# Kernel optimization log

Measured on AMD Instinct MI355X. Metric: run time of the kernel, lower is better.

## Reference

```python
import jax, jax.numpy as jnp
import numpy as np

B, Hh, Ww, D = 16, 32, 32, 1024
NH, HD = 16, 64
S = Hh * Ww


def _rotate_pairwise(x):
    # (..., d) -> pairwise rotation: (x0,x1,x2,x3,...) -> (-x1,x0,-x3,x2,...)
    x = x.reshape(*x.shape[:-1], -1, 2)
    x1, x2 = x[..., 0], x[..., 1]
    return jnp.stack((-x2, x1), axis=-1).reshape(*x.shape[:-2], -1)


def setup_inputs() -> dict:
    key = jax.random.key(0)
    ks = jax.random.split(key, 12)
    s = 1.0 / np.sqrt(D)
    return {
        "hidden_states": jax.random.normal(ks[0], (B, Hh, Ww, D), jnp.float32),
        "cos": jax.random.uniform(ks[1], (S, HD), jnp.float32, -1.0, 1.0),
        "sin": jax.random.uniform(ks[2], (S, HD), jnp.float32, -1.0, 1.0),
        "Wq": jax.random.normal(ks[3], (D, D), jnp.float32) * s,
        "bq": jnp.zeros((D,), jnp.float32),
        "Wk": jax.random.normal(ks[4], (D, D), jnp.float32) * s,
        "bk": jnp.zeros((D,), jnp.float32),
        "Wv": jax.random.normal(ks[5], (D, D), jnp.float32) * s,
        "bv": jnp.zeros((D,), jnp.float32),
        "Wo": jax.random.normal(ks[6], (D, D), jnp.float32) * s,
        "bo": jnp.zeros((D,), jnp.float32),
    }


def reference(hidden_states, cos, sin, Wq, bq, Wk, bk, Wv, bv, Wo, bo):
    b, h, w, d = hidden_states.shape
    seq = h * w
    x = hidden_states.reshape(b, seq, d)
    # QKV projections -> (b, heads, seq, head_dim)
    def proj(W, bias):
        y = x @ W.T + bias
        return y.reshape(b, seq, NH, HD).transpose(0, 2, 1, 3)
    q, k, v = proj(Wq, bq), proj(Wk, bk), proj(Wv, bv)
    # RoPE in fp32; cos/sin (seq, head_dim) broadcast over (b, heads)
    qf = q.astype(jnp.float32)
    kf = k.astype(jnp.float32)
    q = (qf * cos + _rotate_pairwise(qf) * sin).astype(q.dtype)
    k = (kf * cos + _rotate_pairwise(kf) * sin).astype(k.dtype)
    # SDPA
    scale = HD ** -0.5
    scores = jnp.einsum("bhqd,bhkd->bhqk", q, k) * scale
    attn = jax.nn.softmax(scores, axis=-1)
    out = jnp.einsum("bhqk,bhkd->bhqd", attn, v)
    out = out.transpose(0, 2, 1, 3).reshape(b, h, w, d)
    return out @ Wo.T + bo
```

## Files before the change

kernel.cpp:

```cpp
#include <hip/hip_runtime.h>
#include <hip/hip_bf16.h>
#include <stdint.h>

#define Bb 16
#define Ss 1024
#define Dd 1024
#define NHh 16
#define HDd 64
#define Mm 16384

typedef _Float16 half8 __attribute__((ext_vector_type(8)));
typedef float f32x4 __attribute__((ext_vector_type(4)));

__device__ __forceinline__ void gload_lds16(const _Float16* g, _Float16* l) {
  auto* gp = (const __attribute__((address_space(1))) unsigned int*)(g);
  auto* lp = (__attribute__((address_space(3))) unsigned int*)(l);
  __builtin_amdgcn_global_load_lds(gp, lp, 16, 0, 0);
}

__global__ void cast_all(const float* __restrict__ x,
                         const float* __restrict__ wq, const float* __restrict__ wk,
                         const float* __restrict__ wv, const float* __restrict__ wo,
                         _Float16* __restrict__ xh, _Float16* __restrict__ wcat) {
  const long NX = (long)Mm * Dd / 4;
  const long NW = (long)Dd * Dd / 4;
  long c = (long)blockIdx.x * blockDim.x + threadIdx.x;
  const float* src;
  _Float16* dst;
  long o;
  if (c < NX) {
    src = x; o = c; dst = xh;
  } else {
    long cw = c - NX;
    int m = (int)(cw / NW);
    o = cw - (long)m * NW;
    src = (m == 0) ? wq : (m == 1) ? wk : (m == 2) ? wv : wo;
    dst = wcat + (long)m * (Dd * Dd);
  }
  float4 v = reinterpret_cast<const float4*>(src)[o];
  _Float16 h[4] = {(_Float16)v.x, (_Float16)v.y, (_Float16)v.z, (_Float16)v.w};
  reinterpret_cast<uint64_t*>(dst)[o] = *reinterpret_cast<uint64_t*>(h);
}

template <int EPI>
__global__ __launch_bounds__(256, 2) void gemm_nt(
    const _Float16* __restrict__ A, const _Float16* __restrict__ Bm,
    _Float16* __restrict__ qo, _Float16* __restrict__ ko, _Float16* __restrict__ vo,
    const float* __restrict__ bq, const float* __restrict__ bk, const float* __restrict__ bv,
    const float* __restrict__ cosp, const float* __restrict__ sinp,
    float* __restrict__ outp, const float* __restrict__ bo) {
  __shared__ __align__(16) _Float16 As[128 * 32];
  __shared__ __align__(16) _Float16 Bs[128 * 32];
  const int t = threadIdx.x;
  const int w = t >> 6, l = t & 63;
  const int g = l >> 4, ln = l & 15;
  const int wr = w >> 1, wc = w & 1;
  const long rowbase = (long)blockIdx.y * 128;
  const long colbase = (long)blockIdx.x * 128;
  const _Float16* Arow0 = A + rowbase * Dd;
  const _Float16* Brow0 = Bm + colbase * Dd;

  f32x4 acc[4][4];
#pragma unroll
  for (int i = 0; i < 4; ++i)
#pragma unroll
    for (int j = 0; j < 4; ++j) acc[i][j] = f32x4{0.f, 0.f, 0.f, 0.f};

  for (int kt = 0; kt < 32; ++kt) {
    const int kof = kt * 32;
#pragma unroll
    for (int h = 0; h < 2; ++h) {
      int chunk = t + h * 256;
      int r = chunk >> 2;
      int cc = (chunk & 3) * 8;
      gload_lds16(Arow0 + (long)r * Dd + kof + cc, &As[chunk * 8]);
      gload_lds16(Brow0 + (long)r * Dd + kof + cc, &Bs[chunk * 8]);
    }
    __syncthreads();
    half8 af[4], bf[4];
#pragma unroll
    for (int i = 0; i < 4; ++i) {
      af[i] = *reinterpret_cast<const half8*>(&As[(wr * 64 + i * 16 + ln) * 32 + g * 8]);
      bf[i] = *reinterpret_cast<const half8*>(&Bs[(wc * 64 + i * 16 + ln) * 32 + g * 8]);
    }
#pragma unroll
    for (int i = 0; i < 4; ++i)
#pragma unroll
      for (int j = 0; j < 4; ++j)
        acc[i][j] = __builtin_amdgcn_mfma_f32_16x16x32_f16(af[i], bf[j], acc[i][j], 0, 0, 0);
    __syncthreads();
  }

  if (EPI == 0) {
#pragma unroll
    for (int j = 0; j < 4; ++j) {
      long n = colbase + wc * 64 + j * 16 + ln;
      int mat = (int)(n >> 10);
      int col = (int)(n & 1023);
      int hh = col >> 6, hd = col & 63;
      float bias = (mat == 0) ? bq[col] : (mat == 1) ? bk[col] : bv[col];
      _Float16* dst = (mat == 0) ? qo : (mat == 1) ? ko : vo;
#pragma unroll
      for (int i = 0; i < 4; ++i) {
#pragma unroll
        for (int r = 0; r < 4; ++r) {
          long row = rowbase + wr * 64 + i * 16 + g * 4 + r;
          int b = (int)(row >> 10), s = (int)(row & 1023);
          float val = acc[i][j][r] + bias;
          if (mat < 2) {
            float part = __shfl_xor(val, 1);
            float cv = cosp[s * HDd + hd];
            float sv = sinp[s * HDd + hd];
            val = val * cv + ((hd & 1) ? part : -part) * sv;
          }
          dst[((long)(b * NHh + hh) * Ss + s) * HDd + hd] = (_Float16)val;
        }
      }
    }
  } else {
#pragma unroll
    for (int j = 0; j < 4; ++j) {
      long n = colbase + wc * 64 + j * 16 + ln;
      float bias = bo[n];
#pragma unroll
      for (int i = 0; i < 4; ++i)
#pragma unroll
        for (int r = 0; r < 4; ++r) {
          long row = rowbase + wr * 64 + i * 16 + g * 4 + r;
          outp[row * Dd + n] = acc[i][j][r] + bias;
        }
    }
  }
}

__global__ __launch_bounds__(256, 2) void attn(
    const _Float16* __restrict__ Q, const _Float16* __restrict__ K,
    const _Float16* __restrict__ V, _Float16* __restrict__ O) {
  __shared__ __align__(16) _Float16 Ks[64 * 72];
  __shared__ __align__(16) _Float16 Vt[64 * 72];
  __shared__ __align__(16) _Float16 Ps[4 * 16 * 72];
  const int t = threadIdx.x;
  const int w = t >> 6, l = t & 63;
  const int g = l >> 4, ln = l & 15;
  const int pair = blockIdx.y;
  const int qbase = blockIdx.x * 64;
  const long pbase = (long)pair * Ss * HDd;
  const float scale = 0.125f;

  half8 qf[2];
  {
    long qr = qbase + w * 16 + ln;
    const _Float16* qp = Q + pbase + qr * HDd + g * 8;
    qf[0] = *reinterpret_cast<const half8*>(qp);
    qf[1] = *reinterpret_cast<const half8*>(qp + 32);
  }

  float m_i = -1e30f, l_i = 0.0f;
  f32x4 acc_o[4];
#pragma unroll
  for (int c = 0; c < 4; ++c) acc_o[c] = f32x4{0.f, 0.f, 0.f, 0.f};

  for (int kt = 0; kt < 16; ++kt) {
#pragma unroll
    for (int h2 = 0; h2 < 2; ++h2) {
      int chunk = t + h2 * 256;
      int r = chunk >> 3;
      int cc = (chunk & 7) * 8;
      const _Float16* kp = K + pbase + (long)(kt * 64 + r) * HDd + cc;
      half8 kv = *reinterpret_cast<const half8*>(kp);
      *reinterpret_cast<half8*>(&Ks[r * 72 + cc]) = kv;
      const _Float16* vp = V + pbase + (long)(kt * 64 + r) * HDd + cc;
      half8 vv = *reinterpret_cast<const half8*>(vp);
#pragma unroll
      for (int jj = 0; jj < 8; ++jj) Vt[(cc + jj) * 72 + r] = vv[jj];
    }
    __syncthreads();

    f32x4 accs[4];
#pragma unroll
    for (int c = 0; c < 4; ++c) {
      half8 kf0 = *reinterpret_cast<const half8*>(&Ks[(c * 16 + ln) * 72 + g * 8]);
      half8 kf1 = *reinterpret_cast<const half8*>(&Ks[(c * 16 + ln) * 72 + 32 + g * 8]);
      f32x4 a = f32x4{0.f, 0.f, 0.f, 0.f};
      a = __builtin_amdgcn_mfma_f32_16x16x32_f16(kf0, qf[0], a, 0, 0, 0);
      a = __builtin_amdgcn_mfma_f32_16x16x32_f16(kf1, qf[1], a, 0, 0, 0);
      accs[c] = a;
    }

    float pv[16];
    float pmax = -1e30f;
#pragma unroll
    for (int c = 0; c < 4; ++c)
#pragma unroll
      for (int r = 0; r < 4; ++r) {
        float sv = accs[c][r] * scale;
        pv[c * 4 + r] = sv;
        pmax = fmaxf(pmax, sv);
      }
    pmax = fmaxf(pmax, __shfl_xor(pmax, 16));
    pmax = fmaxf(pmax, __shfl_xor(pmax, 32));
    float m_new = fmaxf(m_i, pmax);
    float alpha = __expf(m_i - m_new);
    float tsum = 0.0f;
#pragma unroll
    for (int z = 0; z < 16; ++z) {
      float e = __expf(pv[z] - m_new);
      pv[z] = e;
      tsum += e;
    }
    tsum += __shfl_xor(tsum, 16);
    tsum += __shfl_xor(tsum, 32);
    l_i = l_i * alpha + tsum;
    m_i = m_new;

    float alr[4];
#pragma unroll
    for (int r = 0; r < 4; ++r) alr[r] = __shfl(alpha, g * 4 + r);
#pragma unroll
    for (int c = 0; c < 4; ++c)
#pragma unroll
      for (int r = 0; r < 4; ++r) acc_o[c][r] *= alr[r];

    _Float16* prow = &Ps[(w * 16 + ln) * 72];
#pragma unroll
    for (int c = 0; c < 4; ++c) {
      _Float16 p4[4] = {(_Float16)pv[c * 4 + 0], (_Float16)pv[c * 4 + 1],
                        (_Float16)pv[c * 4 + 2], (_Float16)pv[c * 4 + 3]};
      *reinterpret_cast<uint2*>(&prow[c * 16 + g * 4]) = *reinterpret_cast<uint2*>(p4);
    }

#pragma unroll
    for (int kh = 0; kh < 2; ++kh) {
      half8 pf = *reinterpret_cast<const half8*>(&Ps[(w * 16 + ln) * 72 + kh * 32 + g * 8]);
#pragma unroll
      for (int c = 0; c < 4; ++c) {
        half8 vf = *reinterpret_cast<const half8*>(&Vt[(c * 16 + ln) * 72 + kh * 32 + g * 8]);
        acc_o[c] = __builtin_amdgcn_mfma_f32_16x16x32_f16(pf, vf, acc_o[c], 0, 0, 0);
      }
    }
    __syncthreads();
  }

  const int b = pair >> 4, hh = pair & 15;
  float linv[4];
#pragma unroll
  for (int r = 0; r < 4; ++r) linv[r] = 1.0f / __shfl(l_i, g * 4 + r);
#pragma unroll
  for (int c = 0; c < 4; ++c)
#pragma unroll
    for (int r = 0; r < 4; ++r) {
      int s = qbase + w * 16 + g * 4 + r;
      long addr = ((long)(b * Ss + s)) * Dd + hh * HDd + c * 16 + ln;
      O[addr] = (_Float16)(acc_o[c][r] * linv[r]);
    }
}

extern "C" void kernel_launch(void* const* d_in, const int* in_sizes, int n_in,
                              void* d_out, int out_size, void* d_ws, size_t ws_size,
                              hipStream_t stream) {
  (void)in_sizes; (void)n_in; (void)out_size; (void)ws_size;
  const float* x    = (const float*)d_in[0];
  const float* cosp = (const float*)d_in[1];
  const float* sinp = (const float*)d_in[2];
  const float* Wq   = (const float*)d_in[3];
  const float* bq   = (const float*)d_in[4];
  const float* Wk   = (const float*)d_in[5];
  const float* bk   = (const float*)d_in[6];
  const float* Wv   = (const float*)d_in[7];
  const float* bv   = (const float*)d_in[8];
  const float* Wo   = (const float*)d_in[9];
  const float* bo   = (const float*)d_in[10];
  float* out = (float*)d_out;

  char* ws = (char*)d_ws;
  _Float16* xh   = (_Float16*)(ws);
  _Float16* wcat = (_Float16*)(ws + 33554432);
  _Float16* Qb   = (_Float16*)(ws + 41943040);
  _Float16* Kb   = (_Float16*)(ws + 75497472);
  _Float16* Vb   = (_Float16*)(ws + 109051904);

  cast_all<<<dim3(20480), dim3(256), 0, stream>>>(x, Wq, Wk, Wv, Wo, xh, wcat);

  gemm_nt<0><<<dim3(24, 128), dim3(256), 0, stream>>>(
      xh, wcat, Qb, Kb, Vb, bq, bk, bv, cosp, sinp, (float*)nullptr, (const float*)nullptr);

  attn<<<dim3(16, 256), dim3(256), 0, stream>>>(Qb, Kb, Vb, xh);

  gemm_nt<1><<<dim3(8, 128), dim3(256), 0, stream>>>(
      xh, wcat + (long)3072 * 1024, (_Float16*)nullptr, (_Float16*)nullptr, (_Float16*)nullptr,
      (const float*)nullptr, (const float*)nullptr, (const float*)nullptr,
      (const float*)nullptr, (const float*)nullptr, out, bo);
}
```

Measured before the change: 589.6 us.

## Write V pre-transposed from QKV GEMM and use exp2 softmax in attention

The QKV projection epilogue now stores V in a head-dim-major (transposed) layout with packed 4-element stores, so the attention kernel can load V tiles into shared memory with vector stores instead of scalar transposing scatters. Softmax also folds log2(e) into the scale and uses the hardware exp2 directly. This trades strided global writes in the GEMM epilogue for cheaper LDS fills in the attention inner loop.

```diff
diff --git a/kernel.cpp b/kernel.cpp
--- a/kernel.cpp
+++ b/kernel.cpp
@@ -17,6 +17,8 @@
   auto* lp = (__attribute__((address_space(3))) unsigned int*)(l);
   __builtin_amdgcn_global_load_lds(gp, lp, 16, 0, 0);
 }
+
+__device__ __forceinline__ float fexp2(float x) { return __builtin_amdgcn_exp2f(x); }
 
 __global__ void cast_all(const float* __restrict__ x,
                          const float* __restrict__ wq, const float* __restrict__ wk,
@@ -99,21 +101,32 @@
       int col = (int)(n & 1023);
       int hh = col >> 6, hd = col & 63;
       float bias = (mat == 0) ? bq[col] : (mat == 1) ? bk[col] : bv[col];
-      _Float16* dst = (mat == 0) ? qo : (mat == 1) ? ko : vo;
-#pragma unroll
-      for (int i = 0; i < 4; ++i) {
-#pragma unroll
-        for (int r = 0; r < 4; ++r) {
-          long row = rowbase + wr * 64 + i * 16 + g * 4 + r;
-          int b = (int)(row >> 10), s = (int)(row & 1023);
-          float val = acc[i][j][r] + bias;
-          if (mat < 2) {
+      if (mat < 2) {
+        _Float16* dst = (mat == 0) ? qo : ko;
+#pragma unroll
+        for (int i = 0; i < 4; ++i) {
+#pragma unroll
+          for (int r = 0; r < 4; ++r) {
+            long row = rowbase + wr * 64 + i * 16 + g * 4 + r;
+            int b = (int)(row >> 10), s = (int)(row & 1023);
+            float val = acc[i][j][r] + bias;
             float part = __shfl_xor(val, 1);
             float cv = cosp[s * HDd + hd];
             float sv = sinp[s * HDd + hd];
             val = val * cv + ((hd & 1) ? part : -part) * sv;
+            dst[((long)(b * NHh + hh) * Ss + s) * HDd + hd] = (_Float16)val;
           }
-          dst[((long)(b * NHh + hh) * Ss + s) * HDd + hd] = (_Float16)val;
+        }
+      } else {
+#pragma unroll
+        for (int i = 0; i < 4; ++i) {
+          long row0 = rowbase + wr * 64 + i * 16 + g * 4;
+          int b = (int)(row0 >> 10), s = (int)(row0 & 1023);
+          _Float16 p4[4];
+#pragma unroll
+          for (int r = 0; r < 4; ++r) p4[r] = (_Float16)(acc[i][j][r] + bias);
+          long addr = ((long)((b * NHh + hh) * HDd + hd)) * Ss + s;
+          *reinterpret_cast<uint64_t*>(&vo[addr]) = *reinterpret_cast<uint64_t*>(p4);
         }
       }
     }
@@ -135,7 +148,7 @@
 
 __global__ __launch_bounds__(256, 2) void attn(
     const _Float16* __restrict__ Q, const _Float16* __restrict__ K,
-    const _Float16* __restrict__ V, _Float16* __restrict__ O) {
+    const _Float16* __restrict__ Vt_g, _Float16* __restrict__ O) {
   __shared__ __align__(16) _Float16 Ks[64 * 72];
   __shared__ __align__(16) _Float16 Vt[64 * 72];
   __shared__ __align__(16) _Float16 Ps[4 * 16 * 72];
@@ -145,7 +158,7 @@
   const int pair = blockIdx.y;
   const int qbase = blockIdx.x * 64;
   const long pbase = (long)pair * Ss * HDd;
-  const float scale = 0.125f;
+  const float scale2 = 0.125f * 1.44269504088896f;
 
   half8 qf[2];
   {
@@ -167,12 +180,9 @@
       int r = chunk >> 3;
       int cc = (chunk & 7) * 8;
       const _Float16* kp = K + pbase + (long)(kt * 64 + r) * HDd + cc;
-      half8 kv = *reinterpret_cast<const half8*>(kp);
-      *reinterpret_cast<half8*>(&Ks[r * 72 + cc]) = kv;
-      const _Float16* vp = V + pbase + (long)(kt * 64 + r) * HDd + cc;
-      half8 vv = *reinterpret_cast<const half8*>(vp);
-#pragma unroll
-      for (int jj = 0; jj < 8; ++jj) Vt[(cc + jj) * 72 + r] = vv[jj];
+      *reinterpret_cast<half8*>(&Ks[r * 72 + cc]) = *reinterpret_cast<const half8*>(kp);
+      const _Float16* vp = Vt_g + pbase + (long)r * Ss + kt * 64 + cc;
+      *reinterpret_cast<half8*>(&Vt[r * 72 + cc]) = *reinterpret_cast<const half8*>(vp);
     }
     __syncthreads();
 
@@ -193,18 +203,18 @@
     for (int c = 0; c < 4; ++c)
 #pragma unroll
       for (int r = 0; r < 4; ++r) {
-        float sv = accs[c][r] * scale;
+        float sv = accs[c][r] * scale2;
         pv[c * 4 + r] = sv;
         pmax = fmaxf(pmax, sv);
       }
     pmax = fmaxf(pmax, __shfl_xor(pmax, 16));
     pmax = fmaxf(pmax, __shfl_xor(pmax, 32));
     float m_new = fmaxf(m_i, pmax);
-    float alpha = __expf(m_i - m_new);
+    float alpha = fexp2(m_i - m_new);
     float tsum = 0.0f;
 #pragma unroll
     for (int z = 0; z < 16; ++z) {
-      float e = __expf(pv[z] - m_new);
+      float e = fexp2(pv[z] - m_new);
       pv[z] = e;
       tsum += e;
     }
```

Measured after the change: 501.0 us. 15.0% less time.
